# Kernel tuning notes

Measured on AMD Instinct MI355X. Metric: run time of the kernel, lower is better.

## Reference

```python
import jax, jax.numpy as jnp
import numpy as np
from jax import lax

B, C, H, W = 4, 256, 128, 128
NH = 8
HD = C // NH  # 32
K = 7         # toodd(7) -> 7
DIL = 2
NBH = K // 2  # neighborhood radius


def _window_start(i, L, k, d):
    nh = k // 2
    if d <= 1:
        return max(i - nh, 0) + (L - i - nh - 1 if i + nh >= L else 0)
    ni = i - nh * d
    if ni < 0:
        return i % d
    if i + nh * d >= L:
        imodd = i % d
        a = (L // d) * d
        b = L - a
        if imodd < b:
            return L - b + imodd - 2 * nh * d
        return a + imodd - k * d
    return ni


def _pb_start(i, L, k, d):
    nh = k // 2
    if d <= 1:
        return nh + (nh - i if i < nh else 0) + (L - i - 1 - nh if i + nh >= L else 0)
    if i - nh * d < 0:
        return k - 1 - (i // d)
    if i + nh * d >= L:
        return (L - i - 1) // d
    return nh


# [L, K] neighbor indices per axis, and [L] relative-position-bias start offsets
IDX_H = np.array([[_window_start(i, H, K, DIL) + ki * DIL for ki in range(K)] for i in range(H)], dtype=np.int32)
IDX_W = np.array([[_window_start(j, W, K, DIL) + kj * DIL for kj in range(K)] for j in range(W)], dtype=np.int32)
PB_H = np.array([_pb_start(i, H, K, DIL) for i in range(H)], dtype=np.int32)
PB_W = np.array([_pb_start(j, W, K, DIL) for j in range(W)], dtype=np.int32)


def setup_inputs() -> dict:
    key = jax.random.key(0)
    ks = jax.random.split(key, 8)
    gain = 2.0 ** (-2.5)
    x = jax.random.normal(ks[0], (B, C, H, W), jnp.float32)
    # rotary tables in [-1, 1]
    sin = jax.random.uniform(ks[1], (H, W, HD), jnp.float32, minval=-1.0, maxval=1.0)
    cos = jax.random.uniform(ks[2], (H, W, HD), jnp.float32, minval=-1.0, maxval=1.0)
    w_qkv = jax.random.normal(ks[3], (3 * C, C), jnp.float32) * gain * (2.0 / (4 * C)) ** 0.5
    b_qkv = jnp.zeros((3 * C,), jnp.float32)
    w_lepe = jax.random.normal(ks[4], (C, 1, 5, 5), jnp.float32) * 0.02
    b_lepe = jnp.zeros((C,), jnp.float32)
    w_proj = jax.random.normal(ks[5], (C, C), jnp.float32) * gain * (1.0 / C) ** 0.5
    b_proj = jnp.zeros((C,), jnp.float32)
    rpb = jax.random.normal(ks[6], (NH, 2 * K - 1, 2 * K - 1), jnp.float32) * 0.02
    return {"x": x, "sin": sin, "cos": cos, "w_qkv": w_qkv, "b_qkv": b_qkv,
            "w_lepe": w_lepe, "b_lepe": b_lepe, "w_proj": w_proj, "b_proj": b_proj, "rpb": rpb}


def _rotate_every_two(t):
    t1 = t[..., ::2]
    t2 = t[..., 1::2]
    return jnp.stack([-t2, t1], axis=-1).reshape(t.shape)


def _forward(x, sin, cos, w_qkv, b_qkv, w_lepe, b_lepe, w_proj, b_proj, rpb):
    Bx, Cx, Hx, Wx = x.shape
    # 1x1 qkv conv
    qkv = jnp.einsum('oc,bchw->bohw', w_qkv, x) + b_qkv[None, :, None, None]
    v_chan = qkv[:, 2 * Cx:]
    # LePE: depthwise 5x5 conv on v channels
    lepe = lax.conv_general_dilated(v_chan, w_lepe, (1, 1), [(2, 2), (2, 2)],
                                    feature_group_count=Cx,
                                    dimension_numbers=('NCHW', 'OIHW', 'NCHW'))
    lepe = lepe + b_lepe[None, :, None, None]

    def split_heads(t):  # [B, n*c, H, W] -> [B, n, H, W, c]
        return t.reshape(Bx, NH, HD, Hx, Wx).transpose(0, 1, 3, 4, 2)

    q = split_heads(qkv[:, :Cx])
    k = split_heads(qkv[:, Cx:2 * Cx])
    v = split_heads(v_chan)

    q = (q * cos + _rotate_every_two(q) * sin) * (HD ** -0.5)
    k = k * cos + _rotate_every_two(k) * sin

    idx_h = jnp.asarray(IDX_H)
    idx_w = jnp.asarray(IDX_W)
    pb_h = jnp.asarray(PB_H)
    pb_w = jnp.asarray(PB_W)

    # na2d_qk: dilated neighborhood scores + relative position bias
    attn_slices = []
    for ki in range(K):
        kh = jnp.take(k, idx_h[:, ki], axis=2)          # [B,n,H,W,c]
        for kj in range(K):
            khw = jnp.take(kh, idx_w[:, kj], axis=3)    # [B,n,H,W,c]
            s = jnp.einsum('bnhwc,bnhwc->bnhw', q, khw)
            bias = rpb[:, pb_h + ki][:, :, pb_w + kj]    # [n,H,W]
            attn_slices.append(s + bias[None])
    attn = jnp.stack(attn_slices, axis=-1)               # [B,n,H,W,K*K]
    attn = jax.nn.softmax(attn, axis=-1)

    # na2d_av
    out = jnp.zeros_like(v)
    idx = 0
    for ki in range(K):
        vh = jnp.take(v, idx_h[:, ki], axis=2)
        for kj in range(K):
            vhw = jnp.take(vh, idx_w[:, kj], axis=3)
            out = out + attn[..., idx, None] * vhw
            idx += 1

    out = out.transpose(0, 1, 4, 2, 3).reshape(Bx, Cx, Hx, Wx)  # merge heads
    out = out + lepe
    return jnp.einsum('oc,bchw->bohw', w_proj, out) + b_proj[None, :, None, None]


def reference(x, sin, cos, w_qkv, b_qkv, w_lepe, b_lepe, w_proj, b_proj, rpb):
    return _forward(x, sin, cos, w_qkv, b_qkv, w_lepe, b_lepe, w_proj, b_proj, rpb)
```

## Files before the change

### kernel.cpp

```cpp
#include <hip/hip_runtime.h>
#include <cstddef>

#define HW 16384
#define WID 128

typedef __attribute__((ext_vector_type(8))) short short8;
typedef __attribute__((ext_vector_type(4))) float f32x4;

#define GLD4(g, l)                                                        \
    __builtin_amdgcn_global_load_lds(                                     \
        (const __attribute__((address_space(1))) unsigned int*)(g),       \
        (__attribute__((address_space(3))) unsigned int*)(l), 4, 0, 0)

__device__ __forceinline__ int wstart(int i) {
    if (i < 6) return i & 1;
    if (i >= 122) return 114 + (i & 1);
    return i - 6;
}
__device__ __forceinline__ int pbstart(int i) {
    if (i < 6) return 6 - (i >> 1);
    if (i >= 122) return (127 - i) >> 1;
    return 3;
}

__device__ __forceinline__ unsigned short bf16rne(float f) {
    unsigned u = __builtin_bit_cast(unsigned, f);
    u += 0x7FFFu + ((u >> 16) & 1u);
    return (unsigned short)(u >> 16);
}
__device__ __forceinline__ void bsplit(float f, unsigned short& h, unsigned short& l) {
    h = bf16rne(f);
    float hf = __builtin_bit_cast(float, ((unsigned)h) << 16);
    l = bf16rne(f - hf);
}

__global__ __launch_bounds__(256) void pack_t(const float* __restrict__ src, size_t bstr,
                                              unsigned short* __restrict__ dh,
                                              unsigned short* __restrict__ dl) {
    __shared__ float sm[32][260];
    const int p0 = blockIdx.x * 256, c32 = blockIdx.y, b = blockIdx.z;
    const float* s = src + (size_t)b * bstr + (size_t)(c32 * 32) * HW + p0;
    const int t = threadIdx.x;
    const int rr = t >> 3, f = t & 7;
#pragma unroll
    for (int u = 0; u < 8; u++) {
        float4 v = *(const float4*)(s + (size_t)rr * HW + (f + 8 * u) * 4);
        *(float4*)&sm[rr][(f + 8 * u) * 4] = v;
    }
    __syncthreads();
    size_t off = ((size_t)(b * 8 + c32) * HW + p0 + t) * 32;
#pragma unroll
    for (int w = 0; w < 4; w++) {
        short8 vh, vl;
#pragma unroll
        for (int e = 0; e < 8; e++) {
            unsigned short h, lo_;
            bsplit(sm[w * 8 + e][t], h, lo_);
            vh[e] = (short)h;
            vl[e] = (short)lo_;
        }
        *(short8*)&dh[off + w * 8] = vh;
        *(short8*)&dl[off + w * 8] = vl;
    }
}

template <bool QKV>
__global__ __launch_bounds__(256, 2) void gemm_mfma(
    const float* __restrict__ Wm, const unsigned short* __restrict__ xh,
    const unsigned short* __restrict__ xl, const float* __restrict__ bias,
    const float* __restrict__ sinp, const float* __restrict__ cosp,
    float* __restrict__ Y, int NMT, int MT) {
    __shared__ unsigned short As_h[128][40], As_l[128][40];
    __shared__ unsigned short Bs_h[128][40], Bs_l[128][40];
    const int bid = blockIdx.x;
    const int xcd = bid & 7, r = bid >> 3;
    const int mt = r % NMT;
    const int q2 = r / NMT;
    const int nt = xcd * 16 + (q2 & 15);
    const int b = q2 >> 4;
    const int t = threadIdx.x;
    const int lane = t & 63, wid = t >> 6;
    const int wm = wid >> 1, wn = wid & 1;
    const int m0 = mt * 128;

    f32x4 acc[4][4];
#pragma unroll
    for (int i = 0; i < 4; i++)
#pragma unroll
        for (int j = 0; j < 4; j++) acc[i][j] = (f32x4){0.f, 0.f, 0.f, 0.f};

    const int sr = t >> 1, sh = t & 1;
    const float* arow = Wm + (size_t)(m0 + sr) * 256 + sh * 16;
    const unsigned short* bh_b = xh + ((size_t)(b * 8) * HW + (size_t)nt * 128 + sr) * 32 + sh * 16;
    const unsigned short* bl_b = xl + ((size_t)(b * 8) * HW + (size_t)nt * 128 + sr) * 32 + sh * 16;

    for (int ks = 0; ks < 8; ks++) {
        {
            const float* ap = arow + ks * 32;
#pragma unroll
            for (int g = 0; g < 2; g++) {
                float4 f0 = *(const float4*)(ap + g * 8);
                float4 f1 = *(const float4*)(ap + g * 8 + 4);
                float ff[8] = {f0.x, f0.y, f0.z, f0.w, f1.x, f1.y, f1.z, f1.w};
                short8 vh, vl;
#pragma unroll
                for (int e = 0; e < 8; e++) {
                    unsigned short h, lo_;
                    bsplit(ff[e], h, lo_);
                    vh[e] = (short)h;
                    vl[e] = (short)lo_;
                }
                *(short8*)&As_h[sr][sh * 16 + g * 8] = vh;
                *(short8*)&As_l[sr][sh * 16 + g * 8] = vl;
            }
        }
        {
            const unsigned short* bp = bh_b + (size_t)ks * HW * 32;
            const unsigned short* lp = bl_b + (size_t)ks * HW * 32;
            *(short8*)&Bs_h[sr][sh * 16] = *(const short8*)(bp);
            *(short8*)&Bs_h[sr][sh * 16 + 8] = *(const short8*)(bp + 8);
            *(short8*)&Bs_l[sr][sh * 16] = *(const short8*)(lp);
            *(short8*)&Bs_l[sr][sh * 16 + 8] = *(const short8*)(lp + 8);
        }
        __syncthreads();
        const int k8 = (lane >> 4) * 8;
        short8 a_h[4], a_l[4];
#pragma unroll
        for (int mi = 0; mi < 4; mi++) {
            int am = wm * 64 + mi * 16 + (lane & 15);
            a_h[mi] = *(const short8*)&As_h[am][k8];
            a_l[mi] = *(const short8*)&As_l[am][k8];
        }
#pragma unroll
        for (int ni = 0; ni < 4; ni++) {
            int bn = wn * 64 + ni * 16 + (lane & 15);
            short8 b_h = *(const short8*)&Bs_h[bn][k8];
            short8 b_l = *(const short8*)&Bs_l[bn][k8];
#pragma unroll
            for (int mi = 0; mi < 4; mi++) {
                acc[mi][ni] = __builtin_amdgcn_mfma_f32_16x16x32_bf16(a_h[mi], b_h, acc[mi][ni], 0, 0, 0);
                acc[mi][ni] = __builtin_amdgcn_mfma_f32_16x16x32_bf16(a_h[mi], b_l, acc[mi][ni], 0, 0, 0);
                acc[mi][ni] = __builtin_amdgcn_mfma_f32_16x16x32_bf16(a_l[mi], b_h, acc[mi][ni], 0, 0, 0);
            }
        }
        __syncthreads();
    }

    const int col = lane & 15, rq = (lane >> 4) * 4;
    const int s = QKV ? (mt >> 1) : 3;
#pragma unroll
    for (int mi = 0; mi < 4; mi++) {
        int mrow = m0 + wm * 64 + mi * 16 + rq;
        float b0 = bias[mrow], b1 = bias[mrow + 1], b2 = bias[mrow + 2], b3 = bias[mrow + 3];
#pragma unroll
        for (int ni = 0; ni < 4; ni++) {
            int p = nt * 128 + wn * 64 + ni * 16 + col;
            float v0 = acc[mi][ni][0] + b0, v1 = acc[mi][ni][1] + b1;
            float v2 = acc[mi][ni][2] + b2, v3 = acc[mi][ni][3] + b3;
            if (QKV && s < 2) {
                int d0 = (mi & 1) * 16 + rq;
                const float* cp = cosp + (size_t)p * 32 + d0;
                const float* sp = sinp + (size_t)p * 32 + d0;
                float c0 = cp[0], c1 = cp[1], c2 = cp[2], c3 = cp[3];
                float s0 = sp[0], s1 = sp[1], s2 = sp[2], s3 = sp[3];
                float n0 = v0 * c0 - v1 * s0, n1 = v1 * c1 + v0 * s1;
                float n2 = v2 * c2 - v3 * s2, n3 = v3 * c3 + v2 * s3;
                if (s == 0) {
                    const float sc = 0.17677669529663687f;
                    n0 *= sc; n1 *= sc; n2 *= sc; n3 *= sc;
                }
                v0 = n0; v1 = n1; v2 = n2; v3 = n3;
            }
            float* yp = Y + ((size_t)b * MT + mrow) * HW + p;
            yp[0] = v0;
            yp[HW] = v1;
            yp[2 * HW] = v2;
            yp[3 * HW] = v3;
        }
    }
}

#define CBUF 2048
__global__ __launch_bounds__(256) void attn_k(const float* __restrict__ qkv,
                                              const float* __restrict__ rpb,
                                              const float* __restrict__ wl,
                                              const float* __restrict__ bl,
                                              float* __restrict__ out) {
    __shared__ float sm[2 * CBUF];
    const int t = threadIdx.x;
    const int ty = t >> 7;
    const int j = t & 127;
    const int i0 = blockIdx.x * 2;
    const int i = i0 + ty;
    const int n = blockIdx.y, b = blockIdx.z;
    const int r0 = wstart(i0);
    const int w64 = (t >> 6) * 64;

    const float* qb = qkv + ((size_t)b * 768 + n * 32) * HW;
    const float* kb = qb + (size_t)256 * HW;
    const float* vb = qb + (size_t)512 * HW;
    const int p = i * WID + j;
    const float* qrow = qb + i0 * WID;
    const float* krow = kb + r0 * WID;
    const float* vrow = vb + r0 * WID;

    const int hs = wstart(i), ws_ = wstart(j);
    const int ph = pbstart(i), pw = pbstart(j);

    float sc[49];
    const float* rp = rpb + n * 169;
#pragma unroll
    for (int ki = 0; ki < 7; ki++)
#pragma unroll
        for (int kj = 0; kj < 7; kj++)
            sc[ki * 7 + kj] = rp[(ph + ki) * 13 + (pw + kj)];

    const int aoff = (hs - r0) * WID + ws_;

#pragma unroll
    for (int u = 0; u < 7; u++) GLD4(krow + u * 256 + t, &sm[u * 256 + w64]);
    GLD4(qrow + t, &sm[1792 + w64]);

    for (int c = 0; c < 32; c++) {
        float* bc = sm + (c & 1) * CBUF;
        float* bnx = sm + ((c + 1) & 1) * CBUF;
        if (c < 31) {
            const float* kp = krow + (size_t)(c + 1) * HW;
#pragma unroll
            for (int u = 0; u < 7; u++) GLD4(kp + u * 256 + t, &bnx[u * 256 + w64]);
            GLD4(qrow + (size_t)(c + 1) * HW + t, &bnx[1792 + w64]);
            asm volatile("s_waitcnt vmcnt(8)" ::: "memory");
        } else {
#pragma unroll
            for (int u = 0; u < 7; u++) GLD4(vrow + u * 256 + t, &bnx[u * 256 + w64]);
            asm volatile("s_waitcnt vmcnt(7)" ::: "memory");
        }
        __builtin_amdgcn_s_barrier();
        float qc = bc[1792 + t];
        const float* smb = bc + aoff;
#pragma unroll
        for (int ki = 0; ki < 7; ki++) {
            const float* kib = smb + ki * 256;
#pragma unroll
            for (int kj = 0; kj < 7; kj++)
                sc[ki * 7 + kj] = fmaf(qc, kib[kj * 2], sc[ki * 7 + kj]);
        }
        __builtin_amdgcn_s_barrier();
    }

    float mx = sc[0];
#pragma unroll
    for (int u = 1; u < 49; u++) mx = fmaxf(mx, sc[u]);
    float sum = 0.0f;
#pragma unroll
    for (int u = 0; u < 49; u++) {
        sc[u] = __expf(sc[u] - mx);
        sum += sc[u];
    }
    float inv = 1.0f / sum;
#pragma unroll
    for (int u = 0; u < 49; u++) sc[u] *= inv;

    float* ob = out + ((size_t)b * 768 + n * 32) * HW + p;
    const float* wbase = wl + (size_t)(n * 32) * 25;
    const float* blb = bl + n * 32;
    for (int c = 0; c < 32; c++) {
        float* bc = sm + (c & 1) * CBUF;
        float* bnx = sm + ((c + 1) & 1) * CBUF;
        if (c < 31) {
            const float* vp = vrow + (size_t)(c + 1) * HW;
#pragma unroll
            for (int u = 0; u < 7; u++) GLD4(vp + u * 256 + t, &bnx[u * 256 + w64]);
            asm volatile("s_waitcnt vmcnt(7)" ::: "memory");
        } else {
            asm volatile("s_waitcnt vmcnt(0)" ::: "memory");
        }
        __builtin_amdgcn_s_barrier();
        const float* smb = bc + aoff;
        float oc = 0.0f;
#pragma unroll
        for (int ki = 0; ki < 7; ki++) {
            const float* kib = smb + ki * 256;
#pragma unroll
            for (int kj = 0; kj < 7; kj++)
                oc = fmaf(sc[ki * 7 + kj], kib[kj * 2], oc);
        }
        const float* wrow = wbase + c * 25;
        float lac = blb[c];
#pragma unroll
        for (int di = 0; di < 5; di++) {
            int ii = i + di - 2;
            if ((unsigned)ii < 128u) {
                const float* srow = bc + (ii - r0) * WID;
                const float* wr = wrow + di * 5;
#pragma unroll
                for (int dj = 0; dj < 5; dj++) {
                    int jj = j + dj - 2;
                    if ((unsigned)jj < 128u)
                        lac = fmaf(wr[dj], srow[jj], lac);
                }
            }
        }
        ob[(size_t)c * HW] = oc + lac;
        __builtin_amdgcn_s_barrier();
    }
}

extern "C" void kernel_launch(void* const* d_in, const int* in_sizes, int n_in,
                              void* d_out, int out_size, void* d_ws, size_t ws_size,
                              hipStream_t stream) {
    const float* x = (const float*)d_in[0];
    const float* sinp = (const float*)d_in[1];
    const float* cosp = (const float*)d_in[2];
    const float* w_qkv = (const float*)d_in[3];
    const float* b_qkv = (const float*)d_in[4];
    const float* w_lepe = (const float*)d_in[5];
    const float* b_lepe = (const float*)d_in[6];
    const float* w_proj = (const float*)d_in[7];
    const float* b_proj = (const float*)d_in[8];
    const float* rpb = (const float*)d_in[9];
    float* out = (float*)d_out;

    unsigned short* xph = (unsigned short*)d_ws;
    unsigned short* xpl = xph + 16777216ull;
    float* qkvb = (float*)(xph + 33554432ull);

    pack_t<<<dim3(64, 8, 4), 256, 0, stream>>>(x, (size_t)256 * HW, xph, xpl);
    gemm_mfma<true><<<dim3(3072), 256, 0, stream>>>(w_qkv, xph, xpl, b_qkv, sinp, cosp,
                                                    qkvb, 6, 768);
    attn_k<<<dim3(64, 8, 4), 256, 0, stream>>>(qkvb, rpb, w_lepe, b_lepe, qkvb);
    pack_t<<<dim3(64, 8, 4), 256, 0, stream>>>(qkvb, (size_t)768 * HW, xph, xpl);
    gemm_mfma<false><<<dim3(1024), 256, 0, stream>>>(w_proj, xph, xpl, b_proj, nullptr, nullptr,
                                                     out, 2, 256);
}
```

Measured before the change: 421.3 us.

## Store QKV channel-pair interleaved and process two channels per attention step

The QKV GEMM epilogue now writes q, k and v into separate planes with adjacent channel pairs interleaved per pixel, using float2 stores. The attention kernel reads float2 pairs so each pipeline step covers two channels, which halves the number of barrier-separated iterations. Each block now covers 4 rows with 512 threads and a larger double-buffered LDS tile, and the kernel raises wave priority during compute. The workspace is reorganised so the attention output and the packed buffers alias different regions, which creates buffer-reuse hazards between kernels that must be checked.

Result: slower. 1.389 ms (+229.6%).

```diff
diff --git a/kernel.cpp b/kernel.cpp
--- a/kernel.cpp
+++ b/kernel.cpp
@@ -69,7 +69,7 @@
     const float* __restrict__ Wm, const unsigned short* __restrict__ xh,
     const unsigned short* __restrict__ xl, const float* __restrict__ bias,
     const float* __restrict__ sinp, const float* __restrict__ cosp,
-    float* __restrict__ Y, int NMT, int MT) {
+    float* __restrict__ Y, int NMT) {
     __shared__ unsigned short As_h[128][40], As_l[128][40];
     __shared__ unsigned short Bs_h[128][40], Bs_l[128][40];
     const int bid = blockIdx.x;
@@ -157,52 +157,62 @@
             int p = nt * 128 + wn * 64 + ni * 16 + col;
             float v0 = acc[mi][ni][0] + b0, v1 = acc[mi][ni][1] + b1;
             float v2 = acc[mi][ni][2] + b2, v3 = acc[mi][ni][3] + b3;
-            if (QKV && s < 2) {
-                int d0 = (mi & 1) * 16 + rq;
-                const float* cp = cosp + (size_t)p * 32 + d0;
-                const float* sp = sinp + (size_t)p * 32 + d0;
-                float c0 = cp[0], c1 = cp[1], c2 = cp[2], c3 = cp[3];
-                float s0 = sp[0], s1 = sp[1], s2 = sp[2], s3 = sp[3];
-                float n0 = v0 * c0 - v1 * s0, n1 = v1 * c1 + v0 * s1;
-                float n2 = v2 * c2 - v3 * s2, n3 = v3 * c3 + v2 * s3;
-                if (s == 0) {
-                    const float sc = 0.17677669529663687f;
-                    n0 *= sc; n1 *= sc; n2 *= sc; n3 *= sc;
+            if (QKV) {
+                if (s < 2) {
+                    int d0 = (mi & 1) * 16 + rq;
+                    const float* cp = cosp + (size_t)p * 32 + d0;
+                    const float* sp = sinp + (size_t)p * 32 + d0;
+                    float c0 = cp[0], c1 = cp[1], c2 = cp[2], c3 = cp[3];
+                    float s0 = sp[0], s1 = sp[1], s2 = sp[2], s3 = sp[3];
+                    float n0 = v0 * c0 - v1 * s0, n1 = v1 * c1 + v0 * s1;
+                    float n2 = v2 * c2 - v3 * s2, n3 = v3 * c3 + v2 * s3;
+                    if (s == 0) {
+                        const float sc = 0.17677669529663687f;
+                        n0 *= sc; n1 *= sc; n2 *= sc; n3 *= sc;
+                    }
+                    v0 = n0; v1 = n1; v2 = n2; v3 = n3;
                 }
-                v0 = n0; v1 = n1; v2 = n2; v3 = n3;
-            }
-            float* yp = Y + ((size_t)b * MT + mrow) * HW + p;
-            yp[0] = v0;
-            yp[HW] = v1;
-            yp[2 * HW] = v2;
-            yp[3 * HW] = v3;
-        }
-    }
-}
-
-#define CBUF 2048
-__global__ __launch_bounds__(256) void attn_k(const float* __restrict__ qkv,
-                                              const float* __restrict__ rpb,
-                                              const float* __restrict__ wl,
-                                              const float* __restrict__ bl,
-                                              float* __restrict__ out) {
+                int cloc = mrow & 255;
+                float* dst = Y + (size_t)s * 16777216ull +
+                             ((size_t)(b * 128 + (cloc >> 1))) * 32768ull + (size_t)p * 2;
+                float2 w0 = {v0, v1}, w1 = {v2, v3};
+                *(float2*)dst = w0;
+                *(float2*)(dst + 32768) = w1;
+            } else {
+                float* yp = Y + ((size_t)b * 256 + mrow) * HW + p;
+                yp[0] = v0;
+                yp[HW] = v1;
+                yp[2 * HW] = v2;
+                yp[3 * HW] = v3;
+            }
+        }
+    }
+}
+
+#define CBUF 4096
+__global__ __launch_bounds__(512, 8) void attn_k(const float* __restrict__ qkv2,
+                                                 const float* __restrict__ rpb,
+                                                 const float* __restrict__ wl,
+                                                 const float* __restrict__ bl,
+                                                 float* __restrict__ outp) {
     __shared__ float sm[2 * CBUF];
     const int t = threadIdx.x;
     const int ty = t >> 7;
     const int j = t & 127;
-    const int i0 = blockIdx.x * 2;
-    const int i = i0 + ty;
-    const int n = blockIdx.y, b = blockIdx.z;
+    const int thi = t >> 8;
+    const int tcol = t & 255;
+    const int bid = blockIdx.x;
+    const int it = bid & 31, nb = bid >> 5;
+    const int n = nb & 7, b = nb >> 3;
+    const int i0 = it * 4, i = i0 + ty;
     const int r0 = wstart(i0);
-    const int w64 = (t >> 6) * 64;
-
-    const float* qb = qkv + ((size_t)b * 768 + n * 32) * HW;
-    const float* kb = qb + (size_t)256 * HW;
-    const float* vb = qb + (size_t)512 * HW;
+    const int wbase = (t >> 6) * 64;
+
+    const int pb = b * 128 + n * 16;
+    const float* q2 = qkv2;
+    const float* k2 = qkv2 + 16777216ull;
+    const float* v2 = qkv2 + 33554432ull;
     const int p = i * WID + j;
-    const float* qrow = qb + i0 * WID;
-    const float* krow = kb + r0 * WID;
-    const float* vrow = vb + r0 * WID;
 
     const int hs = wstart(i), ws_ = wstart(j);
     const int ph = pbstart(i), pw = pbstart(j);
@@ -215,36 +225,56 @@
         for (int kj = 0; kj < 7; kj++)
             sc[ki * 7 + kj] = rp[(ph + ki) * 13 + (pw + kj)];
 
-    const int aoff = (hs - r0) * WID + ws_;
-
-#pragma unroll
-    for (int u = 0; u < 7; u++) GLD4(krow + u * 256 + t, &sm[u * 256 + w64]);
-    GLD4(qrow + t, &sm[1792 + w64]);
-
-    for (int c = 0; c < 32; c++) {
-        float* bc = sm + (c & 1) * CBUF;
-        float* bnx = sm + ((c + 1) & 1) * CBUF;
-        if (c < 31) {
-            const float* kp = krow + (size_t)(c + 1) * HW;
-#pragma unroll
-            for (int u = 0; u < 7; u++) GLD4(kp + u * 256 + t, &bnx[u * 256 + w64]);
-            GLD4(qrow + (size_t)(c + 1) * HW + t, &bnx[1792 + w64]);
+    const int lrbase = hs - r0;
+    const int abase = lrbase * 256 + ws_ * 2;
+
+    {
+        const float* kpl = k2 + (size_t)pb * 32768ull;
+#pragma unroll
+        for (int u = 0; u < 8; u++) {
+            int row = r0 + 2 * u + thi; if (row > 127) row = 127;
+            GLD4(kpl + row * 256 + tcol, &sm[u * 512 + wbase]);
+        }
+    }
+    float2 qv = *(const float2*)(q2 + (size_t)pb * 32768ull + (size_t)p * 2);
+    float2 qn;
+
+    for (int cp = 0; cp < 16; cp++) {
+        float* bc = sm + (cp & 1) * CBUF;
+        float* bnx = sm + ((cp + 1) & 1) * CBUF;
+        if (cp < 15) {
+            const float* kpl = k2 + (size_t)(pb + cp + 1) * 32768ull;
+#pragma unroll
+            for (int u = 0; u < 8; u++) {
+                int row = r0 + 2 * u + thi; if (row > 127) row = 127;
+                GLD4(kpl + row * 256 + tcol, &bnx[u * 512 + wbase]);
+            }
+            qn = *(const float2*)(q2 + (size_t)(pb + cp + 1) * 32768ull + (size_t)p * 2);
+            asm volatile("s_waitcnt vmcnt(9)" ::: "memory");
+        } else {
+            const float* vpl = v2 + (size_t)pb * 32768ull;
+#pragma unroll
+            for (int u = 0; u < 8; u++) {
+                int row = r0 + 2 * u + thi; if (row > 127) row = 127;
+                GLD4(vpl + row * 256 + tcol, &bnx[u * 512 + wbase]);
+            }
             asm volatile("s_waitcnt vmcnt(8)" ::: "memory");
-        } else {
-#pragma unroll
-            for (int u = 0; u < 7; u++) GLD4(vrow + u * 256 + t, &bnx[u * 256 + w64]);
-            asm volatile("s_waitcnt vmcnt(7)" ::: "memory");
         }
         __builtin_amdgcn_s_barrier();
-        float qc = bc[1792 + t];
-        const float* smb = bc + aoff;
+        __builtin_amdgcn_s_setprio(1);
+        const float* ab = bc + abase;
 #pragma unroll
         for (int ki = 0; ki < 7; ki++) {
-            const float* kib = smb + ki * 256;
-#pragma unroll
-            for (int kj = 0; kj < 7; kj++)
-                sc[ki * 7 + kj] = fmaf(qc, kib[kj * 2], sc[ki * 7 + kj]);
-        }
+            const float* kib = ab + ki * 512;
+#pragma unroll
+            for (int kj = 0; kj < 7; kj++) {
+                float2 tp = *(const float2*)(kib + kj * 4);
+                sc[ki * 7 + kj] = fmaf(qv.x, tp.x, sc[ki * 7 + kj]);
+                sc[ki * 7 + kj] = fmaf(qv.y, tp.y, sc[ki * 7 + kj]);
+            }
+        }
+        __builtin_amdgcn_s_setprio(0);
+        qv = qn;
         __builtin_amdgcn_s_barrier();
     }
 
@@ -261,47 +291,61 @@
 #pragma unroll
     for (int u = 0; u < 49; u++) sc[u] *= inv;
 
-    float* ob = out + ((size_t)b * 768 + n * 32) * HW + p;
-    const float* wbase = wl + (size_t)(n * 32) * 25;
+    float* ob = outp + ((size_t)(b * 256 + n * 32) * HW) + p;
+    const float* wbaseL = wl + (size_t)(n * 32) * 25;
     const float* blb = bl + n * 32;
-    for (int c = 0; c < 32; c++) {
-        float* bc = sm + (c & 1) * CBUF;
-        float* bnx = sm + ((c + 1) & 1) * CBUF;
-        if (c < 31) {
-            const float* vp = vrow + (size_t)(c + 1) * HW;
-#pragma unroll
-            for (int u = 0; u < 7; u++) GLD4(vp + u * 256 + t, &bnx[u * 256 + w64]);
-            asm volatile("s_waitcnt vmcnt(7)" ::: "memory");
+    for (int cp = 0; cp < 16; cp++) {
+        float* bc = sm + (cp & 1) * CBUF;
+        float* bnx = sm + ((cp + 1) & 1) * CBUF;
+        if (cp < 15) {
+            const float* vpl = v2 + (size_t)(pb + cp + 1) * 32768ull;
+#pragma unroll
+            for (int u = 0; u < 8; u++) {
+                int row = r0 + 2 * u + thi; if (row > 127) row = 127;
+                GLD4(vpl + row * 256 + tcol, &bnx[u * 512 + wbase]);
+            }
+            asm volatile("s_waitcnt vmcnt(8)" ::: "memory");
         } else {
             asm volatile("s_waitcnt vmcnt(0)" ::: "memory");
         }
         __builtin_amdgcn_s_barrier();
-        const float* smb = bc + aoff;
-        float oc = 0.0f;
+        __builtin_amdgcn_s_setprio(1);
+        const float* ab = bc + abase;
+        float oc0 = 0.0f, oc1 = 0.0f;
 #pragma unroll
         for (int ki = 0; ki < 7; ki++) {
-            const float* kib = smb + ki * 256;
-#pragma unroll
-            for (int kj = 0; kj < 7; kj++)
-                oc = fmaf(sc[ki * 7 + kj], kib[kj * 2], oc);
-        }
-        const float* wrow = wbase + c * 25;
-        float lac = blb[c];
+            const float* kib = ab + ki * 512;
+#pragma unroll
+            for (int kj = 0; kj < 7; kj++) {
+                float2 tp = *(const float2*)(kib + kj * 4);
+                float w = sc[ki * 7 + kj];
+                oc0 = fmaf(w, tp.x, oc0);
+                oc1 = fmaf(w, tp.y, oc1);
+            }
+        }
+        const int ch = 2 * cp;
+        const float* w0 = wbaseL + ch * 25;
+        const float* w1 = w0 + 25;
+        float la0 = blb[ch], la1 = blb[ch + 1];
 #pragma unroll
         for (int di = 0; di < 5; di++) {
             int ii = i + di - 2;
             if ((unsigned)ii < 128u) {
-                const float* srow = bc + (ii - r0) * WID;
-                const float* wr = wrow + di * 5;
+                const float* srow = bc + (ii - r0) * 256;
 #pragma unroll
                 for (int dj = 0; dj < 5; dj++) {
                     int jj = j + dj - 2;
-                    if ((unsigned)jj < 128u)
-                        lac = fmaf(wr[dj], srow[jj], lac);
+                    if ((unsigned)jj < 128u) {
+                        float2 tp = *(const float2*)(srow + jj * 2);
+                        la0 = fmaf(w0[di * 5 + dj], tp.x, la0);
+                        la1 = fmaf(w1[di * 5 + dj], tp.y, la1);
+                    }
                 }
             }
         }
-        ob[(size_t)c * HW] = oc + lac;
+        __builtin_amdgcn_s_setprio(0);
+        ob[(size_t)ch * HW] = oc0 + la0;
+        ob[(size_t)(ch + 1) * HW] = oc1 + la1;
         __builtin_amdgcn_s_barrier();
     }
 }
@@ -321,15 +365,19 @@
     const float* rpb = (const float*)d_in[9];
     float* out = (float*)d_out;
 
-    unsigned short* xph = (unsigned short*)d_ws;
-    unsigned short* xpl = xph + 16777216ull;
-    float* qkvb = (float*)(xph + 33554432ull);
-
-    pack_t<<<dim3(64, 8, 4), 256, 0, stream>>>(x, (size_t)256 * HW, xph, xpl);
-    gemm_mfma<true><<<dim3(3072), 256, 0, stream>>>(w_qkv, xph, xpl, b_qkv, sinp, cosp,
-                                                    qkvb, 6, 768);
-    attn_k<<<dim3(64, 8, 4), 256, 0, stream>>>(qkvb, rpb, w_lepe, b_lepe, qkvb);
-    pack_t<<<dim3(64, 8, 4), 256, 0, stream>>>(qkvb, (size_t)768 * HW, xph, xpl);
-    gemm_mfma<false><<<dim3(1024), 256, 0, stream>>>(w_proj, xph, xpl, b_proj, nullptr, nullptr,
-                                                     out, 2, 256);
-}
+    float* wsf = (float*)d_ws;
+    float* qkv2 = wsf;
+    float* attno = wsf + 50331648ull;
+    unsigned short* xph_in = (unsigned short*)attno;
+    unsigned short* xpl_in = xph_in + 16777216ull;
+    unsigned short* xph2 = (unsigned short*)wsf;
+    unsigned short* xpl2 = xph2 + 16777216ull;
+
+    pack_t<<<dim3(64, 8, 4), 256, 0, stream>>>(x, (size_t)256 * HW, xph_in, xpl_in);
+    gemm_mfma<true><<<dim3(3072), 256, 0, stream>>>(w_qkv, xph_in, xpl_in, b_qkv, sinp, cosp,
+                                                    qkv2, 6);
+    attn_k<<<dim3(1024), 512, 0, stream>>>(qkv2, rpb, w_lepe, b_lepe, attno);
+    pack_t<<<dim3(64, 8, 4), 256, 0, stream>>>(attno, (size_t)256 * HW, xph2, xpl2);
+    gemm_mfma<false><<<dim3(1024), 256, 0, stream>>>(w_proj, xph2, xpl2, b_proj, nullptr, nullptr,
+                                                     out, 2);
+}
```

## Process two channels per pipeline stage in attention kernel and swizzle row blocks

Applied to the files above, without the earlier changes.

The attention kernel's double-buffered LDS pipeline now stages two channels per step instead of one. This halves the number of barriers and keeps more global-to-LDS loads in flight. It also remaps blockIdx.x with a bit permutation so neighbouring blocks handle spread-out row pairs, and raises wave priority with s_setprio during the compute sections. In exchange, LDS use per block doubles, which may reduce how many blocks fit on each CU.

Measured after the change: 406.7 us. 1.04x faster.

```diff
diff --git a/kernel.cpp b/kernel.cpp
--- a/kernel.cpp
+++ b/kernel.cpp
@@ -180,17 +180,20 @@
     }
 }
 
-#define CBUF 2048
+#define CW 2048
+#define PBUF 4096
 __global__ __launch_bounds__(256) void attn_k(const float* __restrict__ qkv,
                                               const float* __restrict__ rpb,
                                               const float* __restrict__ wl,
                                               const float* __restrict__ bl,
                                               float* __restrict__ out) {
-    __shared__ float sm[2 * CBUF];
+    __shared__ float sm[2 * PBUF];
     const int t = threadIdx.x;
     const int ty = t >> 7;
     const int j = t & 127;
-    const int i0 = blockIdx.x * 2;
+    const int bx = blockIdx.x;
+    const int ip = ((bx & 7) << 3) | (bx >> 3);
+    const int i0 = ip * 2;
     const int i = i0 + ty;
     const int n = blockIdx.y, b = blockIdx.z;
     const int r0 = wstart(i0);
@@ -218,33 +221,51 @@
     const int aoff = (hs - r0) * WID + ws_;
 
 #pragma unroll
-    for (int u = 0; u < 7; u++) GLD4(krow + u * 256 + t, &sm[u * 256 + w64]);
-    GLD4(qrow + t, &sm[1792 + w64]);
-
-    for (int c = 0; c < 32; c++) {
-        float* bc = sm + (c & 1) * CBUF;
-        float* bnx = sm + ((c + 1) & 1) * CBUF;
-        if (c < 31) {
-            const float* kp = krow + (size_t)(c + 1) * HW;
-#pragma unroll
-            for (int u = 0; u < 7; u++) GLD4(kp + u * 256 + t, &bnx[u * 256 + w64]);
-            GLD4(qrow + (size_t)(c + 1) * HW + t, &bnx[1792 + w64]);
-            asm volatile("s_waitcnt vmcnt(8)" ::: "memory");
+    for (int s = 0; s < 2; s++) {
+        const float* kp = krow + (size_t)s * HW;
+#pragma unroll
+        for (int u = 0; u < 7; u++) GLD4(kp + u * 256 + t, &sm[s * CW + u * 256 + w64]);
+        GLD4(qrow + (size_t)s * HW + t, &sm[s * CW + 1792 + w64]);
+    }
+
+    for (int cp = 0; cp < 16; cp++) {
+        float* bc = sm + (cp & 1) * PBUF;
+        float* bnx = sm + ((cp + 1) & 1) * PBUF;
+        if (cp < 15) {
+#pragma unroll
+            for (int s = 0; s < 2; s++) {
+                const int c = 2 * (cp + 1) + s;
+                const float* kp = krow + (size_t)c * HW;
+#pragma unroll
+                for (int u = 0; u < 7; u++) GLD4(kp + u * 256 + t, &bnx[s * CW + u * 256 + w64]);
+                GLD4(qrow + (size_t)c * HW + t, &bnx[s * CW + 1792 + w64]);
+            }
+            asm volatile("s_waitcnt vmcnt(16)" ::: "memory");
         } else {
 #pragma unroll
-            for (int u = 0; u < 7; u++) GLD4(vrow + u * 256 + t, &bnx[u * 256 + w64]);
-            asm volatile("s_waitcnt vmcnt(7)" ::: "memory");
+            for (int s = 0; s < 2; s++) {
+                const float* vp = vrow + (size_t)s * HW;
+#pragma unroll
+                for (int u = 0; u < 7; u++) GLD4(vp + u * 256 + t, &bnx[s * CW + u * 256 + w64]);
+            }
+            asm volatile("s_waitcnt vmcnt(14)" ::: "memory");
         }
         __builtin_amdgcn_s_barrier();
-        float qc = bc[1792 + t];
-        const float* smb = bc + aoff;
-#pragma unroll
-        for (int ki = 0; ki < 7; ki++) {
-            const float* kib = smb + ki * 256;
-#pragma unroll
-            for (int kj = 0; kj < 7; kj++)
-                sc[ki * 7 + kj] = fmaf(qc, kib[kj * 2], sc[ki * 7 + kj]);
-        }
+        __builtin_amdgcn_s_setprio(1);
+#pragma unroll
+        for (int s = 0; s < 2; s++) {
+            const float* bs = bc + s * CW;
+            float qc = bs[1792 + t];
+            const float* smb = bs + aoff;
+#pragma unroll
+            for (int ki = 0; ki < 7; ki++) {
+                const float* kib = smb + ki * 256;
+#pragma unroll
+                for (int kj = 0; kj < 7; kj++)
+                    sc[ki * 7 + kj] = fmaf(qc, kib[kj * 2], sc[ki * 7 + kj]);
+            }
+        }
+        __builtin_amdgcn_s_setprio(0);
         __builtin_amdgcn_s_barrier();
     }
 
@@ -264,44 +285,55 @@
     float* ob = out + ((size_t)b * 768 + n * 32) * HW + p;
     const float* wbase = wl + (size_t)(n * 32) * 25;
     const float* blb = bl + n * 32;
-    for (int c = 0; c < 32; c++) {
-        float* bc = sm + (c & 1) * CBUF;
-        float* bnx = sm + ((c + 1) & 1) * CBUF;
-        if (c < 31) {
-            const float* vp = vrow + (size_t)(c + 1) * HW;
-#pragma unroll
-            for (int u = 0; u < 7; u++) GLD4(vp + u * 256 + t, &bnx[u * 256 + w64]);
-            asm volatile("s_waitcnt vmcnt(7)" ::: "memory");
+    for (int cp = 0; cp < 16; cp++) {
+        float* bc = sm + (cp & 1) * PBUF;
+        float* bnx = sm + ((cp + 1) & 1) * PBUF;
+        if (cp < 15) {
+#pragma unroll
+            for (int s = 0; s < 2; s++) {
+                const int c = 2 * (cp + 1) + s;
+                const float* vp = vrow + (size_t)c * HW;
+#pragma unroll
+                for (int u = 0; u < 7; u++) GLD4(vp + u * 256 + t, &bnx[s * CW + u * 256 + w64]);
+            }
+            asm volatile("s_waitcnt vmcnt(14)" ::: "memory");
         } else {
             asm volatile("s_waitcnt vmcnt(0)" ::: "memory");
         }
         __builtin_amdgcn_s_barrier();
-        const float* smb = bc + aoff;
-        float oc = 0.0f;
-#pragma unroll
-        for (int ki = 0; ki < 7; ki++) {
-            const float* kib = smb + ki * 256;
-#pragma unroll
-            for (int kj = 0; kj < 7; kj++)
-                oc = fmaf(sc[ki * 7 + kj], kib[kj * 2], oc);
-        }
-        const float* wrow = wbase + c * 25;
-        float lac = blb[c];
-#pragma unroll
-        for (int di = 0; di < 5; di++) {
-            int ii = i + di - 2;
-            if ((unsigned)ii < 128u) {
-                const float* srow = bc + (ii - r0) * WID;
-                const float* wr = wrow + di * 5;
-#pragma unroll
-                for (int dj = 0; dj < 5; dj++) {
-                    int jj = j + dj - 2;
-                    if ((unsigned)jj < 128u)
-                        lac = fmaf(wr[dj], srow[jj], lac);
+        __builtin_amdgcn_s_setprio(1);
+#pragma unroll
+        for (int s = 0; s < 2; s++) {
+            const int ch = 2 * cp + s;
+            const float* bs = bc + s * CW;
+            const float* smb = bs + aoff;
+            float oc = 0.0f;
+#pragma unroll
+            for (int ki = 0; ki < 7; ki++) {
+                const float* kib = smb + ki * 256;
+#pragma unroll
+                for (int kj = 0; kj < 7; kj++)
+                    oc = fmaf(sc[ki * 7 + kj], kib[kj * 2], oc);
+            }
+            const float* wrow = wbase + ch * 25;
+            float lac = blb[ch];
+#pragma unroll
+            for (int di = 0; di < 5; di++) {
+                int ii = i + di - 2;
+                if ((unsigned)ii < 128u) {
+                    const float* srow = bs + (ii - r0) * WID;
+                    const float* wr = wrow + di * 5;
+#pragma unroll
+                    for (int dj = 0; dj < 5; dj++) {
+                        int jj = j + dj - 2;
+                        if ((unsigned)jj < 128u)
+                            lac = fmaf(wr[dj], srow[jj], lac);
+                    }
                 }
             }
-        }
-        ob[(size_t)c * HW] = oc + lac;
+            ob[(size_t)ch * HW] = oc + lac;
+        }
+        __builtin_amdgcn_s_setprio(0);
         __builtin_amdgcn_s_barrier();
     }
 }
```
